# Performance work log

Measured on AMD Instinct MI355X. Metric: run time of the kernel, lower is better.

The kernel has to match this reference:

```python
import jax, jax.numpy as jnp
import numpy as np

L, B, IN, H, OUT = 4, 4096, 1024, 1024, 1024


def setup_inputs() -> dict:
    key = jax.random.key(0)
    ks = jax.random.split(key, 9)
    std = 1.0 / (H + IN) ** 0.5
    return {
        "x": jax.random.normal(ks[0], (B, IN), jnp.float32),
        "h_prev": jax.random.normal(ks[1], (L, B, H), jnp.float32),
        "c_prev": jax.random.normal(ks[2], (L, B, H), jnp.float32),
        "Wi": jax.random.uniform(ks[3], (L, IN, 4 * H), jnp.float32, -std, std),
        "Wh": jax.random.uniform(ks[4], (L, H, 4 * H), jnp.float32, -std, std),
        "bi": jax.random.uniform(ks[5], (L, 4 * H), jnp.float32, -std, std),
        "bh": jax.random.uniform(ks[6], (L, 4 * H), jnp.float32, -std, std),
        "fc_W": jax.random.uniform(ks[7], (H, OUT), jnp.float32, -std, std),
        "fc_b": jax.random.uniform(ks[8], (OUT,), jnp.float32, -std, std),
    }


def _lstm_cell(x, h, c, Wi, Wh, bi, bh):
    # gates: [B, 4H], split into (input, forget, cell, output)
    gates = x @ Wi + bi + h @ Wh + bh
    i, f, g, o = jnp.split(gates, 4, axis=1)
    i, f, o = jax.nn.sigmoid(i), jax.nn.sigmoid(f), jax.nn.sigmoid(o)
    g = jnp.tanh(g)
    c_cur = f * c + i * g
    h_cur = o * jnp.tanh(c_cur)
    return h_cur, c_cur


def reference(x, h_prev, c_prev, Wi, Wh, bi, bh, fc_W, fc_b):
    h_out, c_out = [], []
    x_in = x
    for l in range(L):  # fixed small layer loop
        h_cur, c_cur = _lstm_cell(x_in, h_prev[l], c_prev[l], Wi[l], Wh[l], bi[l], bh[l])
        h_out.append(h_cur)
        c_out.append(c_cur)
        x_in = h_cur
    h_out = jnp.stack(h_out, axis=0)
    c_out = jnp.stack(c_out, axis=0)
    y = h_out[-1] @ fc_W + fc_b
    return y, h_out, c_out
```

## Files before the change

kernel.cpp:

```cpp
#include <hip/hip_runtime.h>

#define B_    4096
#define H_    1024
#define NLAY  4

typedef __attribute__((ext_vector_type(8))) short bf16x8;
typedef __attribute__((ext_vector_type(4))) short s16x4;
typedef __attribute__((ext_vector_type(4))) float f32x4;
typedef unsigned short ushort_t;

__device__ __forceinline__ ushort_t f2bf(float f) {
  unsigned u = __builtin_bit_cast(unsigned, f);
  u += 0x7FFFu + ((u >> 16) & 1u);
  return (ushort_t)(u >> 16);
}

__device__ __forceinline__ float fast_sigmoid(float x) {
  float e = __expf(-fabsf(x));
  float s = 1.0f / (1.0f + e);
  return x >= 0.0f ? s : 1.0f - s;
}
__device__ __forceinline__ float fast_tanh(float x) {
  float e = __expf(-2.0f * fabsf(x));
  float t = (1.0f - e) / (1.0f + e);
  return x >= 0.0f ? t : -t;
}

#define GLDS16(gsrc, ldst)                                                  \
  __builtin_amdgcn_global_load_lds(                                         \
      (__attribute__((address_space(1))) void*)(gsrc),                      \
      (__attribute__((address_space(3))) void*)(ldst), 16, 0, 0)

#define BAR()                                                               \
  { asm volatile("" ::: "memory");                                          \
    __builtin_amdgcn_s_barrier();                                           \
    asm volatile("" ::: "memory"); }

#define WAITV(N)                                                            \
  { asm volatile("s_waitcnt vmcnt(" #N ")" ::: "memory");                   \
    __builtin_amdgcn_sched_barrier(0); }

#define LGKM0()                                                             \
  { asm volatile("s_waitcnt lgkmcnt(0)" ::: "memory");                      \
    __builtin_amdgcn_sched_barrier(0); }

__device__ __forceinline__ bf16x8 dsr128(unsigned addr, int imm) {
  bf16x8 r;
  asm volatile("ds_read_b128 %0, %1 offset:%c2"
               : "=v"(r)
               : "v"(addr), "i"(imm));
  return r;
}

__global__ __launch_bounds__(512, 1) void lstm8(
    const ushort_t* __restrict__ aX, const ushort_t* __restrict__ aH,
    const float* __restrict__ cprev, const float* __restrict__ bi,
    const float* __restrict__ bh, const ushort_t* __restrict__ wtl,
    float* __restrict__ hout, float* __restrict__ cout,
    ushort_t* __restrict__ hbfout) {
  __shared__ __align__(16) char sL[131072];

  const int tid  = threadIdx.x;
  const int lane = tid & 63;
  const int wid  = tid >> 6;
  const int wm   = wid >> 2;
  const int wn   = wid & 3;
  const int bid  = (blockIdx.x & 7) * 32 + (blockIdx.x >> 3);
  const int bm   = bid & 15;
  const int bn   = bid >> 4;

  const int fr = lane & 15;
  const int oF = lane >> 4;
  const int sw = (oF ^ ((fr >> 1) & 3)) * 16;

  const unsigned sBase = (unsigned)(size_t)&sL[0];
  const unsigned aAddr = sBase + (unsigned)(wm * 16384 + fr * 64 + sw);
  const unsigned bAddr = sBase + (unsigned)(65536 + (wn >> 1) * 16384 +
                                            (wn & 1) * 4096 + fr * 64 + sw);

  const int oA = (tid & 3) ^ ((tid >> 3) & 3);
  const size_t aOff0 = (size_t)(bm * 256 + (tid >> 2)) * 1024 + oA * 8;
  const size_t aOff1 = aOff0 + (size_t)128 * 1024;
  const ushort_t* wtBn = wtl + (size_t)bn * 524288;

  f32x4 acc[8][4];
#pragma unroll
  for (int m = 0; m < 8; ++m)
#pragma unroll
    for (int g = 0; g < 4; ++g) acc[m][g] = (f32x4){0.f, 0.f, 0.f, 0.f};

  bf16x8 ar[4][2], br0[2][2], br1[2][2];

#define STAGE_A(PAR, HALF, TT)                                               \
  {                                                                          \
    const ushort_t* s0 =                                                     \
        (((TT) < 16) ? aX : aH) + ((HALF) ? aOff1 : aOff0) + ((TT) & 15) * 64; \
    char* d = sL + (PAR) * 32768 + (HALF) * 16384 + wid * 1024;              \
    GLDS16(s0, d);                                                           \
    GLDS16(s0 + 32, d + 8192);                                               \
  }
#define STAGE_B(PAR, HALF, TT)                                               \
  {                                                                          \
    const ushort_t* s0 =                                                     \
        wtBn + (size_t)((TT) & 31) * 16384 + (HALF) * 8192 + tid * 8;        \
    char* d = sL + 65536 + (PAR) * 32768 + (HALF) * 16384 + wid * 1024;      \
    GLDS16(s0, d);                                                           \
    GLDS16(s0 + 4096, d + 8192);                                             \
  }
#define RD_A(PAR, MH)                                                        \
  _Pragma("unroll") for (int mp = 0; mp < 4; ++mp)                           \
      _Pragma("unroll") for (int kh = 0; kh < 2; ++kh)                       \
      ar[mp][kh] = dsr128(aAddr, (PAR) * 32768 + kh * 8192 +                 \
                                     ((MH) * 4 + mp) * 1024);
#define RD_B(PAR, NH, BR)                                                    \
  _Pragma("unroll") for (int gg = 0; gg < 2; ++gg)                           \
      _Pragma("unroll") for (int kh = 0; kh < 2; ++kh)                       \
      BR[gg][kh] = dsr128(bAddr, (PAR) * 32768 + kh * 8192 +                 \
                                     ((NH) * 2 + gg) * 1024);
#define MM(MH, NH, BR)                                                       \
  __builtin_amdgcn_s_setprio(1);                                             \
  _Pragma("unroll") for (int gg = 0; gg < 2; ++gg)                           \
      _Pragma("unroll") for (int mp = 0; mp < 4; ++mp)                       \
      _Pragma("unroll") for (int kh = 0; kh < 2; ++kh)                       \
      acc[(MH) * 4 + mp][(NH) * 2 + gg] =                                    \
          __builtin_amdgcn_mfma_f32_16x16x32_bf16(                           \
              ar[mp][kh], BR[gg][kh], acc[(MH) * 4 + mp][(NH) * 2 + gg],     \
              0, 0, 0);                                                      \
  __builtin_amdgcn_s_setprio(0);

  STAGE_A(0, 0, 0)
  STAGE_A(0, 1, 0)
  STAGE_B(0, 0, 0)
  STAGE_B(0, 1, 0)
  STAGE_B(1, 0, 1)
  STAGE_B(1, 1, 1)
  WAITV(4)
  BAR()

#pragma unroll 1
  for (int t2 = 0; t2 < 32; t2 += 2) {
    RD_A(0, 0) RD_B(0, 0, br0)
    STAGE_A(1, 0, t2 + 1)
    BAR()
    LGKM0()
    MM(0, 0, br0)
    BAR()

    RD_B(0, 1, br1)
    STAGE_A(1, 1, t2 + 1)
    BAR()
    LGKM0()
    MM(0, 1, br1)
    BAR()

    RD_A(0, 1)
    STAGE_B(0, 0, (t2 + 2))
    BAR()
    LGKM0()
    MM(1, 0, br0)
    BAR()

    STAGE_B(0, 1, (t2 + 2))
    BAR()
    MM(1, 1, br1)
    WAITV(4)
    BAR()

    RD_A(1, 0) RD_B(1, 0, br0)
    STAGE_A(0, 0, (t2 + 2))
    BAR()
    LGKM0()
    MM(0, 0, br0)
    BAR()

    RD_B(1, 1, br1)
    STAGE_A(0, 1, (t2 + 2))
    BAR()
    LGKM0()
    MM(0, 1, br1)
    BAR()

    RD_A(1, 1)
    STAGE_B(1, 0, (t2 + 3))
    BAR()
    LGKM0()
    MM(1, 0, br0)
    BAR()

    STAGE_B(1, 1, (t2 + 3))
    BAR()
    MM(1, 1, br1)
    WAITV(4)
    BAR()
  }
#undef STAGE_A
#undef STAGE_B
#undef RD_A
#undef RD_B
#undef MM

  WAITV(0)
  __syncthreads();

  const int hcolL = wn * 16 + fr;
  const int hcol  = bn * 64 + hcolL;
  float bsum[4];
#pragma unroll
  for (int g = 0; g < 4; ++g)
    bsum[g] = bi[g * 1024 + hcol] + bh[g * 1024 + hcol];

#define LSTRIDE 68
  float* LF = (float*)sL;
  const int crow = tid >> 4;
  const int cc4  = (tid & 15) * 4;
  {
    const float* cp0 = cprev + (size_t)(bm * 256) * 1024 + bn * 64;
#pragma unroll
    for (int i = 0; i < 8; ++i) {
      const int row = i * 32 + crow;
      f32x4 v = *(const f32x4*)(cp0 + (size_t)row * 1024 + cc4);
      *(f32x4*)(LF + row * LSTRIDE + cc4) = v;
    }
  }
  __syncthreads();
  float cv[8][4], hv[8][4];
#pragma unroll
  for (int m = 0; m < 8; ++m) {
    const int rowb = wm * 128 + m * 16 + oF * 4;
#pragma unroll
    for (int r = 0; r < 4; ++r) {
      const float cp = LF[(rowb + r) * LSTRIDE + hcolL];
      const float gi = fast_sigmoid(acc[m][0][r] + bsum[0]);
      const float gf = fast_sigmoid(acc[m][1][r] + bsum[1]);
      const float gg = fast_tanh(acc[m][2][r] + bsum[2]);
      const float go = fast_sigmoid(acc[m][3][r] + bsum[3]);
      const float c  = gf * cp + gi * gg;
      cv[m][r] = c;
      hv[m][r] = go * fast_tanh(c);
    }
  }
  __syncthreads();
#pragma unroll
  for (int m = 0; m < 8; ++m) {
    const int rowb = wm * 128 + m * 16 + oF * 4;
#pragma unroll
    for (int r = 0; r < 4; ++r) LF[(rowb + r) * LSTRIDE + hcolL] = cv[m][r];
  }
  __syncthreads();
  {
    float* co0 = cout + (size_t)(bm * 256) * 1024 + bn * 64;
#pragma unroll
    for (int i = 0; i < 8; ++i) {
      const int row = i * 32 + crow;
      f32x4 v = *(const f32x4*)(LF + row * LSTRIDE + cc4);
      *(f32x4*)(co0 + (size_t)row * 1024 + cc4) = v;
    }
  }
  __syncthreads();
#pragma unroll
  for (int m = 0; m < 8; ++m) {
    const int rowb = wm * 128 + m * 16 + oF * 4;
#pragma unroll
    for (int r = 0; r < 4; ++r) LF[(rowb + r) * LSTRIDE + hcolL] = hv[m][r];
  }
  __syncthreads();
  {
    float* ho0 = hout + (size_t)(bm * 256) * 1024 + bn * 64;
    ushort_t* hb0 = hbfout + (size_t)(bm * 256) * 1024 + bn * 64;
#pragma unroll
    for (int i = 0; i < 8; ++i) {
      const int row = i * 32 + crow;
      f32x4 v = *(const f32x4*)(LF + row * LSTRIDE + cc4);
      *(f32x4*)(ho0 + (size_t)row * 1024 + cc4) = v;
      s16x4 hb;
#pragma unroll
      for (int j = 0; j < 4; ++j) hb[j] = (short)f2bf(v[j]);
      *(s16x4*)(hb0 + (size_t)row * 1024 + cc4) = hb;
    }
  }
#undef LSTRIDE
}

__global__ __launch_bounds__(512) void packW(const float* __restrict__ Wi,
                                             const float* __restrict__ Wh,
                                             ushort_t* __restrict__ wt) {
  __shared__ ushort_t t16[64 * 256];
  const int bn = blockIdx.x;
  const int T  = blockIdx.y;
  const int l  = blockIdx.z;
  const int tid = threadIdx.x;
  const int kq = tid >> 6, cc = tid & 63;
  const int k0 = T * 64;
  const float* W = (k0 < 1024)
                       ? (Wi + (size_t)l * 1024 * 4096 + (size_t)k0 * 4096)
                       : (Wh + (size_t)l * 1024 * 4096 + (size_t)(k0 - 1024) * 4096);
#pragma unroll
  for (int kk = 0; kk < 8; ++kk) {
    const int kl = kq * 8 + kk;
#pragma unroll
    for (int g = 0; g < 4; ++g) {
      const float v = W[(size_t)kl * 4096 + g * 1024 + bn * 64 + cc];
      const int p = (cc >> 4) * 64 + g * 16 + (cc & 15);
      t16[kl * 256 + p] = f2bf(v);
    }
  }
  __syncthreads();
#pragma unroll
  for (int half = 0; half < 2; ++half) {
    ushort_t* img =
        wt + (((size_t)l * 16 + bn) * 32 + T) * 16384 + half * 8192;
#pragma unroll
    for (int c = 0; c < 2; ++c) {
      const int idx = c * 512 + tid;
      const int kh = idx >> 9;
      const int r  = (idx >> 2) & 127;
      const int s  = idx & 3;
      const int o  = s ^ ((r >> 1) & 3);
      const int klb = kh * 32 + o * 8;
      const int pg  = half * 128 + r;
      bf16x8 ov;
#pragma unroll
      for (int j = 0; j < 8; ++j) ov[j] = (short)t16[(klb + j) * 256 + pg];
      *(bf16x8*)(img + (size_t)idx * 8) = ov;
    }
  }
}

__device__ __forceinline__ int swz(int row, int kelem) {
  return ((row * 64 + kelem) * 2) ^ ((row & 7) << 4);
}

__global__ __launch_bounds__(512) void fc_kernel(
    const ushort_t* __restrict__ wtfc, const ushort_t* __restrict__ abf,
    const float* __restrict__ bias, float* __restrict__ y) {
  __shared__ __align__(16) char sA[128 * 64 * 2];
  __shared__ __align__(16) char sB[64 * 64 * 2];
  const int tid  = threadIdx.x;
  const int lane = tid & 63;
  const int wid  = tid >> 6;
  const int wm   = wid >> 2;
  const int wn   = wid & 3;
  const int bid  = (blockIdx.x & 7) * 64 + (blockIdx.x >> 3);
  const int bm   = bid & 31;
  const int bn   = bid >> 5;

  f32x4 acc[4];
#pragma unroll
  for (int m = 0; m < 4; ++m) acc[m] = (f32x4){0.f, 0.f, 0.f, 0.f};

  const int rloc = wid * 8 + (lane >> 3);
  const int jA   = (lane & 7) ^ ((lane >> 3) & 7);
  const ushort_t* aSrc = abf + (size_t)(bm * 128 + rloc) * 1024 + jA * 8;

  for (int ks = 0; ks < 16; ++ks) {
    __syncthreads();
    GLDS16(wtfc + (size_t)(bn * 16 + ks) * 4096 + tid * 8, sB + wid * 1024);
    const int off = ks * 64;
    GLDS16(aSrc + off,             sA + wid * 1024);
    GLDS16(aSrc + off + 64 * 1024, sA + 8192 + wid * 1024);
    __syncthreads();
#pragma unroll
    for (int kk = 0; kk < 64; kk += 32) {
      const int ke = kk + (lane >> 4) * 8;
      bf16x8 a[4];
#pragma unroll
      for (int m = 0; m < 4; ++m)
        a[m] = *(const bf16x8*)(sA + swz(wm * 64 + m * 16 + (lane & 15), ke));
      bf16x8 b = *(const bf16x8*)(sB + swz(wn * 16 + (lane & 15), ke));
#pragma unroll
      for (int m = 0; m < 4; ++m)
        acc[m] = __builtin_amdgcn_mfma_f32_16x16x32_bf16(a[m], b, acc[m], 0, 0, 0);
    }
  }
  const int col = bn * 64 + wn * 16 + (lane & 15);
  const float bb = bias[col];
#pragma unroll
  for (int m = 0; m < 4; ++m) {
    const int row0 = bm * 128 + wm * 64 + m * 16 + ((lane >> 4) << 2);
#pragma unroll
    for (int r = 0; r < 4; ++r)
      y[(size_t)(row0 + r) * 1024 + col] = acc[m][r] + bb;
  }
}

__global__ __launch_bounds__(512) void transposeFc(const float* __restrict__ W,
                                                   ushort_t* __restrict__ wt) {
  const int bn = blockIdx.x;
  const int ks = blockIdx.y;
  const int tid = threadIdx.x;
  const int c  = tid & 63;
  const int ko = (tid >> 6) * 8;
  float v[8];
#pragma unroll
  for (int j = 0; j < 8; ++j)
    v[j] = W[(size_t)(ks * 64 + ko + j) * 1024 + bn * 64 + c];
  bf16x8 o;
#pragma unroll
  for (int j = 0; j < 8; ++j) o[j] = (short)f2bf(v[j]);
  ushort_t* tile = wt + ((size_t)bn * 16 + ks) * 4096;
  *(bf16x8*)((char*)tile + swz(c, ko)) = o;
}

__global__ __launch_bounds__(256) void cvt_bf16(const float* __restrict__ s,
                                                ushort_t* __restrict__ d,
                                                int n8) {
  const int i = blockIdx.x * 256 + threadIdx.x;
  if (i >= n8) return;
  const float* p = s + (size_t)i * 8;
  f32x4 a = ((const f32x4*)p)[0];
  f32x4 b = ((const f32x4*)p)[1];
  bf16x8 o;
#pragma unroll
  for (int j = 0; j < 4; ++j) {
    o[j]     = (short)f2bf(a[j]);
    o[4 + j] = (short)f2bf(b[j]);
  }
  *(bf16x8*)(d + (size_t)i * 8) = o;
}

extern "C" void kernel_launch(void* const* d_in, const int* in_sizes, int n_in,
                              void* d_out, int out_size, void* d_ws,
                              size_t ws_size, hipStream_t stream) {
  const float* x     = (const float*)d_in[0];
  const float* hprev = (const float*)d_in[1];
  const float* cprev = (const float*)d_in[2];
  const float* Wi    = (const float*)d_in[3];
  const float* Wh    = (const float*)d_in[4];
  const float* bi    = (const float*)d_in[5];
  const float* bh    = (const float*)d_in[6];
  const float* fcW   = (const float*)d_in[7];
  const float* fcb   = (const float*)d_in[8];

  float* out = (float*)d_out;
  const size_t BH = (size_t)B_ * H_;
  float* y    = out;
  float* hout = out + BH;
  float* cout = out + 5 * BH;

  const size_t WT_ELEMS = (size_t)4 * 16 * 32 * 16384;
  const size_t FC_ELEMS = (size_t)16 * 16 * 4096;
  ushort_t* wt      = (ushort_t*)d_ws;
  ushort_t* fcwt    = wt + WT_ELEMS;
  ushort_t* xbf     = fcwt + FC_ELEMS;
  ushort_t* hprevbf = xbf + BH;
  ushort_t* houtbf  = hprevbf + 4 * BH;

  packW<<<dim3(16, 32, 4), dim3(512), 0, stream>>>(Wi, Wh, wt);
  transposeFc<<<dim3(16, 16), dim3(512), 0, stream>>>(fcW, fcwt);
  cvt_bf16<<<dim3((int)(BH / 8 / 256)), dim3(256), 0, stream>>>(x, xbf,
                                                                (int)(BH / 8));
  cvt_bf16<<<dim3((int)(4 * BH / 8 / 256)), dim3(256), 0, stream>>>(
      hprev, hprevbf, (int)(4 * BH / 8));

  for (int l = 0; l < NLAY; ++l) {
    const ushort_t* aX  = (l == 0) ? xbf : (houtbf + (size_t)(l - 1) * BH);
    const ushort_t* wtl = wt + (size_t)l * 16 * 32 * 16384;
    lstm8<<<dim3(256), dim3(512), 0, stream>>>(
        aX, hprevbf + (size_t)l * BH, cprev + (size_t)l * BH, bi + l * 4096,
        bh + l * 4096, wtl, hout + (size_t)l * BH, cout + (size_t)l * BH,
        houtbf + (size_t)l * BH);
  }
  fc_kernel<<<dim3(512), dim3(512), 0, stream>>>(fcwt, houtbf + 3 * BH, fcb, y);
}
```

Measured before the change: 384.5 us.

## Peel last K iterations to prefetch c_prev, pad packW LDS, merge bf16 conversions

Peels the final two K-steps out of the main LSTM GEMM loop so c_prev can be loaded straight from global memory into registers while the last MFMAs run. This removes the separate LDS staging pass and a barrier in the epilogue. packW's shared-memory tile gets a row stride of 257 to reduce bank conflicts, and the two bf16 conversion kernels are merged into one launch. The launch bound hint changes to 2 waves-per-EU, which may constrain register allocation and risk spills given the 128KB LDS and large accumulator arrays.

```diff
diff --git a/kernel.cpp b/kernel.cpp
--- a/kernel.cpp
+++ b/kernel.cpp
@@ -52,7 +52,7 @@
   return r;
 }
 
-__global__ __launch_bounds__(512, 1) void lstm8(
+__global__ __launch_bounds__(512, 2) void lstm8(
     const ushort_t* __restrict__ aX, const ushort_t* __restrict__ aH,
     const float* __restrict__ cprev, const float* __restrict__ bi,
     const float* __restrict__ bh, const ushort_t* __restrict__ wtl,
@@ -138,7 +138,7 @@
   BAR()
 
 #pragma unroll 1
-  for (int t2 = 0; t2 < 32; t2 += 2) {
+  for (int t2 = 0; t2 < 30; t2 += 2) {
     RD_A(0, 0) RD_B(0, 0, br0)
     STAGE_A(1, 0, t2 + 1)
     BAR()
@@ -192,6 +192,66 @@
     MM(1, 1, br1)
     WAITV(4)
     BAR()
+  }
+
+  float cpv[8][4];
+  {
+    RD_A(0, 0) RD_B(0, 0, br0)
+    STAGE_A(1, 0, 31)
+    BAR()
+    LGKM0()
+    MM(0, 0, br0)
+    BAR()
+
+    RD_B(0, 1, br1)
+    STAGE_A(1, 1, 31)
+    BAR()
+    LGKM0()
+    MM(0, 1, br1)
+    BAR()
+
+    RD_A(0, 1)
+    {
+      const float* cpT = cprev +
+                         (size_t)(bm * 256 + wm * 128 + oF * 4) * 1024 +
+                         bn * 64 + wn * 16 + fr;
+#pragma unroll
+      for (int m = 0; m < 8; ++m)
+#pragma unroll
+        for (int r = 0; r < 4; ++r)
+          cpv[m][r] = cpT[(size_t)(m * 16 + r) * 1024];
+    }
+    BAR()
+    LGKM0()
+    MM(1, 0, br0)
+    BAR()
+
+    BAR()
+    MM(1, 1, br1)
+    WAITV(32)
+    BAR()
+
+    RD_A(1, 0) RD_B(1, 0, br0)
+    BAR()
+    LGKM0()
+    MM(0, 0, br0)
+    BAR()
+
+    RD_B(1, 1, br1)
+    BAR()
+    LGKM0()
+    MM(0, 1, br1)
+    BAR()
+
+    RD_A(1, 1)
+    BAR()
+    LGKM0()
+    MM(1, 0, br0)
+    BAR()
+
+    BAR()
+    MM(1, 1, br1)
+    WAITV(0)
   }
 #undef STAGE_A
 #undef STAGE_B
@@ -199,7 +259,6 @@
 #undef RD_B
 #undef MM
 
-  WAITV(0)
   __syncthreads();
 
   const int hcolL = wn * 16 + fr;
@@ -208,38 +267,26 @@
 #pragma unroll
   for (int g = 0; g < 4; ++g)
     bsum[g] = bi[g * 1024 + hcol] + bh[g * 1024 + hcol];
+
+  float cv[8][4], hv[8][4];
+#pragma unroll
+  for (int m = 0; m < 8; ++m) {
+#pragma unroll
+    for (int r = 0; r < 4; ++r) {
+      const float gi = fast_sigmoid(acc[m][0][r] + bsum[0]);
+      const float gf = fast_sigmoid(acc[m][1][r] + bsum[1]);
+      const float gg = fast_tanh(acc[m][2][r] + bsum[2]);
+      const float go = fast_sigmoid(acc[m][3][r] + bsum[3]);
+      const float c  = gf * cpv[m][r] + gi * gg;
+      cv[m][r] = c;
+      hv[m][r] = go * fast_tanh(c);
+    }
+  }
 
 #define LSTRIDE 68
   float* LF = (float*)sL;
   const int crow = tid >> 4;
   const int cc4  = (tid & 15) * 4;
-  {
-    const float* cp0 = cprev + (size_t)(bm * 256) * 1024 + bn * 64;
-#pragma unroll
-    for (int i = 0; i < 8; ++i) {
-      const int row = i * 32 + crow;
-      f32x4 v = *(const f32x4*)(cp0 + (size_t)row * 1024 + cc4);
-      *(f32x4*)(LF + row * LSTRIDE + cc4) = v;
-    }
-  }
-  __syncthreads();
-  float cv[8][4], hv[8][4];
-#pragma unroll
-  for (int m = 0; m < 8; ++m) {
-    const int rowb = wm * 128 + m * 16 + oF * 4;
-#pragma unroll
-    for (int r = 0; r < 4; ++r) {
-      const float cp = LF[(rowb + r) * LSTRIDE + hcolL];
-      const float gi = fast_sigmoid(acc[m][0][r] + bsum[0]);
-      const float gf = fast_sigmoid(acc[m][1][r] + bsum[1]);
-      const float gg = fast_tanh(acc[m][2][r] + bsum[2]);
-      const float go = fast_sigmoid(acc[m][3][r] + bsum[3]);
-      const float c  = gf * cp + gi * gg;
-      cv[m][r] = c;
-      hv[m][r] = go * fast_tanh(c);
-    }
-  }
-  __syncthreads();
 #pragma unroll
   for (int m = 0; m < 8; ++m) {
     const int rowb = wm * 128 + m * 16 + oF * 4;
@@ -284,7 +331,7 @@
 __global__ __launch_bounds__(512) void packW(const float* __restrict__ Wi,
                                              const float* __restrict__ Wh,
                                              ushort_t* __restrict__ wt) {
-  __shared__ ushort_t t16[64 * 256];
+  __shared__ ushort_t t16[64 * 257];
   const int bn = blockIdx.x;
   const int T  = blockIdx.y;
   const int l  = blockIdx.z;
@@ -301,7 +348,7 @@
     for (int g = 0; g < 4; ++g) {
       const float v = W[(size_t)kl * 4096 + g * 1024 + bn * 64 + cc];
       const int p = (cc >> 4) * 64 + g * 16 + (cc & 15);
-      t16[kl * 256 + p] = f2bf(v);
+      t16[kl * 257 + p] = f2bf(v);
     }
   }
   __syncthreads();
@@ -320,7 +367,7 @@
       const int pg  = half * 128 + r;
       bf16x8 ov;
 #pragma unroll
-      for (int j = 0; j < 8; ++j) ov[j] = (short)t16[(klb + j) * 256 + pg];
+      for (int j = 0; j < 8; ++j) ov[j] = (short)t16[(klb + j) * 257 + pg];
       *(bf16x8*)(img + (size_t)idx * 8) = ov;
     }
   }
@@ -401,21 +448,32 @@
   *(bf16x8*)((char*)tile + swz(c, ko)) = o;
 }
 
-__global__ __launch_bounds__(256) void cvt_bf16(const float* __restrict__ s,
-                                                ushort_t* __restrict__ d,
-                                                int n8) {
-  const int i = blockIdx.x * 256 + threadIdx.x;
-  if (i >= n8) return;
-  const float* p = s + (size_t)i * 8;
-  f32x4 a = ((const f32x4*)p)[0];
-  f32x4 b = ((const f32x4*)p)[1];
+__global__ __launch_bounds__(256) void cvt_bf16_2(const float* __restrict__ s0,
+                                                  unsigned n0,
+                                                  const float* __restrict__ s1,
+                                                  ushort_t* __restrict__ d0,
+                                                  ushort_t* __restrict__ d1,
+                                                  unsigned ntot) {
+  const unsigned i = blockIdx.x * 256 + threadIdx.x;
+  if (i >= ntot) return;
+  const float* p;
+  ushort_t* d;
+  unsigned j;
+  if (i < n0) {
+    p = s0; d = d0; j = i;
+  } else {
+    p = s1; d = d1; j = i - n0;
+  }
+  const float* pp = p + (size_t)j * 8;
+  f32x4 a = ((const f32x4*)pp)[0];
+  f32x4 b = ((const f32x4*)pp)[1];
   bf16x8 o;
 #pragma unroll
-  for (int j = 0; j < 4; ++j) {
-    o[j]     = (short)f2bf(a[j]);
-    o[4 + j] = (short)f2bf(b[j]);
-  }
-  *(bf16x8*)(d + (size_t)i * 8) = o;
+  for (int k = 0; k < 4; ++k) {
+    o[k]     = (short)f2bf(a[k]);
+    o[4 + k] = (short)f2bf(b[k]);
+  }
+  *(bf16x8*)(d + (size_t)j * 8) = o;
 }
 
 extern "C" void kernel_launch(void* const* d_in, const int* in_sizes, int n_in,
@@ -447,10 +505,13 @@
 
   packW<<<dim3(16, 32, 4), dim3(512), 0, stream>>>(Wi, Wh, wt);
   transposeFc<<<dim3(16, 16), dim3(512), 0, stream>>>(fcW, fcwt);
-  cvt_bf16<<<dim3((int)(BH / 8 / 256)), dim3(256), 0, stream>>>(x, xbf,
-                                                                (int)(BH / 8));
-  cvt_bf16<<<dim3((int)(4 * BH / 8 / 256)), dim3(256), 0, stream>>>(
-      hprev, hprevbf, (int)(4 * BH / 8));
+  {
+    const unsigned n0 = (unsigned)(BH / 8);
+    const unsigned n1 = (unsigned)(4 * BH / 8);
+    const unsigned nt = n0 + n1;
+    cvt_bf16_2<<<dim3((nt + 255) / 256), dim3(256), 0, stream>>>(
+        x, n0, hprev, xbf, hprevbf, nt);
+  }
 
   for (int l = 0; l < NLAY; ++l) {
     const ushort_t* aX  = (l == 0) ? xbf : (houtbf + (size_t)(l - 1) * BH);
```

After: 408.3 us. 6.2% more time.
